# Kernel optimization log

Hardware: AMD Instinct MI355X
Metric: run time of the kernel (lower is better)

Reference implementation:

```python
import jax, jax.numpy as jnp
import numpy as np

K = 20  # kNN fan-out


def knn_idx(x, k):
    # x: (B, C, N). Negative squared pairwise distance; top-k largest = nearest.
    inner = -2.0 * jnp.einsum('bcn,bcm->bnm', x, x)        # (B, N, N)
    xx = jnp.sum(x * x, axis=1)                            # (B, N)
    pd = -xx[:, :, None] - inner - xx[:, None, :]          # (B, N, N)
    return jax.lax.top_k(pd, k)[1]                         # (B, N, k) int32


def get_graph_feature(x, k):
    # x: (B, C, N) -> edge features (B, 2C, N, k)
    idx = knn_idx(x, k)                                    # (B, N, k)
    xt = jnp.transpose(x, (0, 2, 1))                       # (B, N, C)
    nbrs = jax.vmap(lambda pts, ids: pts[ids])(xt, idx)    # (B, N, k, C)
    center = xt[:, :, None, :]                             # (B, N, 1, C)
    feat = jnp.concatenate(
        [nbrs - center, jnp.broadcast_to(center, nbrs.shape)], axis=-1)  # (B,N,k,2C)
    return jnp.transpose(feat, (0, 3, 1, 2))               # (B, 2C, N, k)


def vn_layer(W, x):
    # W: (out, in); x: (B, in, N, k) -> (B, out, N, k)
    return jnp.einsum('oi,bink->bonk', W, x)


def setup_inputs() -> dict:
    key = jax.random.key(0)
    ks = jax.random.split(key, 6)
    B, C, N = 16, 3, 2048
    num_classes = 10
    return {
        'x': jax.random.normal(ks[0], (B, C, N), dtype=jnp.float32),
        'W1': jax.random.normal(ks[1], (64, 6), dtype=jnp.float32),
        'W2': jax.random.normal(ks[2], (128, 64), dtype=jnp.float32),
        'W3': jax.random.normal(ks[3], (256, 128), dtype=jnp.float32),
        'fc_w': jax.random.normal(ks[4], (num_classes, 256), dtype=jnp.float32) * 0.0625,
        'fc_b': jax.random.normal(ks[5], (num_classes,), dtype=jnp.float32) * 0.0625,
    }


def reference(x, W1, W2, W3, fc_w, fc_b):
    h = get_graph_feature(x, K)          # (B, 6, N, k)
    h = vn_layer(W1, h)                  # (B, 64, N, k)
    h = jax.nn.relu(vn_layer(W2, h))     # (B, 128, N, k)
    h = jax.nn.relu(vn_layer(W3, h))     # (B, 256, N, k)
    h = jnp.max(h, axis=-1)              # max over neighbors k -> (B, 256, N)
    h = jnp.max(h, axis=-1)              # global max over points -> (B, 256)
    return h @ fc_w.T + fc_b             # (B, num_classes)
```

## Files before the change

kernel.cpp:

```cpp
#include <hip/hip_runtime.h>
#include <stdint.h>

typedef _Float16 v8h __attribute__((ext_vector_type(8)));
typedef _Float16 v2h __attribute__((ext_vector_type(2)));
typedef float v4f __attribute__((ext_vector_type(4)));

#define NPTS 2048
#define BATCH 16
#define KNN 20
#define PAIRS (NPTS * KNN)

__device__ __forceinline__ unsigned pair_relu_h2(unsigned pu, unsigned qu) {
  v2h a = *(const v2h*)&pu;
  v2h b = *(const v2h*)&qu;
  v2h s = a + b;
  v2h z = {(_Float16)0.f, (_Float16)0.f};
  v2h r = __builtin_elementwise_max(s, z);
  return *(const unsigned*)&r;
}

__global__ void prep_kernel(const float* __restrict__ W1, const float* __restrict__ W2,
                            float* __restrict__ M2a, float* __restrict__ M2b,
                            int* __restrict__ H) {
  if (blockIdx.x == 0 && threadIdx.x < 128) {
    int o = threadIdx.x;
    float a0 = 0, a1 = 0, a2 = 0, b0 = 0, b1 = 0, b2 = 0;
    for (int i = 0; i < 64; ++i) {
      float w2 = W2[o * 64 + i];
      const float* w1r = W1 + i * 6;
      a0 += w2 * w1r[0]; a1 += w2 * w1r[1]; a2 += w2 * w1r[2];
      b0 += w2 * (w1r[3] - w1r[0]); b1 += w2 * (w1r[4] - w1r[1]); b2 += w2 * (w1r[5] - w1r[2]);
    }
    M2a[o * 3 + 0] = a0; M2a[o * 3 + 1] = a1; M2a[o * 3 + 2] = a2;
    M2b[o * 3 + 0] = b0; M2b[o * 3 + 1] = b1; M2b[o * 3 + 2] = b2;
  }
  int g = blockIdx.x * 128 + threadIdx.x;
  if (g < BATCH * 256) H[g] = 0;
}

__global__ __launch_bounds__(64) void pq_kernel(const float* __restrict__ x,
                                                const float* __restrict__ M2a,
                                                const float* __restrict__ M2b,
                                                unsigned short* __restrict__ p,
                                                unsigned short* __restrict__ q) {
  int b = blockIdx.x >> 6;
  int j0 = (blockIdx.x & 63) << 5;
  int t = threadIdx.x;
  int o0 = t * 2;
  float a00 = M2a[o0 * 3 + 0], a01 = M2a[o0 * 3 + 1], a02 = M2a[o0 * 3 + 2];
  float a10 = M2a[o0 * 3 + 3], a11 = M2a[o0 * 3 + 4], a12 = M2a[o0 * 3 + 5];
  float b00 = M2b[o0 * 3 + 0], b01 = M2b[o0 * 3 + 1], b02 = M2b[o0 * 3 + 2];
  float b10 = M2b[o0 * 3 + 3], b11 = M2b[o0 * 3 + 4], b12 = M2b[o0 * 3 + 5];
  const float* xb = x + b * 3 * NPTS;
  unsigned* pw = (unsigned*)p;
  unsigned* qw = (unsigned*)q;
  for (int jj = 0; jj < 32; ++jj) {
    int j = j0 + jj;
    float x0 = xb[j], x1 = xb[NPTS + j], x2 = xb[2 * NPTS + j];
    float p0 = a00 * x0 + a01 * x1 + a02 * x2;
    float p1 = a10 * x0 + a11 * x1 + a12 * x2;
    float q0 = b00 * x0 + b01 * x1 + b02 * x2;
    float q1 = b10 * x0 + b11 * x1 + b12 * x2;
    size_t base = ((size_t)(b * NPTS + j)) * 64 + t;
    auto hp = __builtin_amdgcn_cvt_pkrtz(p0, p1);
    auto hq = __builtin_amdgcn_cvt_pkrtz(q0, q1);
    pw[base] = *(const unsigned*)&hp;
    qw[base] = *(const unsigned*)&hq;
  }
}

__global__ __launch_bounds__(256) void knn_kernel(const float* __restrict__ x,
                                                  int* __restrict__ idxOut) {
  __shared__ float px[NPTS], py[NPTS], pz[NPTS];
  __shared__ unsigned long long cand[4][4][128];
  int b = blockIdx.x >> 7;
  int qblk = blockIdx.x & 127;
  const float* xb = x + b * 3 * NPTS;
  for (int i = threadIdx.x; i < NPTS; i += 256) {
    px[i] = xb[i]; py[i] = xb[NPTS + i]; pz[i] = xb[2 * NPTS + i];
  }
  __syncthreads();
  int wid = threadIdx.x >> 6, lane = threadIdx.x & 63;
  int qbase = qblk * 16 + wid * 4;

  float qx[4], qy[4], qz[4], mn[4];
#pragma unroll
  for (int g = 0; g < 4; ++g) {
    qx[g] = px[qbase + g]; qy[g] = py[qbase + g]; qz[g] = pz[qbase + g];
    mn[g] = 1e30f;
  }

  for (int s = 0; s < 32; ++s) {
    int i = s * 64 + lane;
    float X = px[i], Y = py[i], Z = pz[i];
#pragma unroll
    for (int g = 0; g < 4; ++g) {
      float dx = X - qx[g], dy = Y - qy[g], dz = Z - qz[g];
      mn[g] = fminf(mn[g], dx * dx + dy * dy + dz * dz);
    }
  }

  float tau[4];
#pragma unroll
  for (int g = 0; g < 4; ++g) {
    float v = mn[g];
    for (int k = 2; k <= 64; k <<= 1) {
      for (int j = k >> 1; j > 0; j >>= 1) {
        float o = __shfl_xor(v, j);
        bool low = (lane & j) == 0;
        bool up = (lane & k) == 0;
        v = (low == up) ? fminf(v, o) : fmaxf(v, o);
      }
    }
    tau[g] = __shfl(v, 19) * (1.0f + 3.8e-6f);
  }

  int cnt[4] = {0, 0, 0, 0};
  for (int s = 0; s < 32; ++s) {
    int i = s * 64 + lane;
    float X = px[i], Y = py[i], Z = pz[i];
#pragma unroll
    for (int g = 0; g < 4; ++g) {
      float dx = X - qx[g], dy = Y - qy[g], dz = Z - qz[g];
      float d = dx * dx + dy * dy + dz * dz;
      bool take = d <= tau[g];
      unsigned long long mb = __ballot(take);
      if (take) {
        int pos = cnt[g] + __popcll(mb & ((1ull << lane) - 1ull));
        if (pos < 128)
          cand[wid][g][pos] =
              (((unsigned long long)__float_as_uint(d)) << 32) | (unsigned)i;
      }
      cnt[g] += __popcll(mb);
    }
  }

#pragma unroll
  for (int g = 0; g < 4; ++g) {
    int nc = cnt[g] < 128 ? cnt[g] : 128;
    unsigned long long k0 = (lane < nc) ? cand[wid][g][lane] : ~0ull;
    unsigned long long k1 = (lane + 64 < nc) ? cand[wid][g][lane + 64] : ~0ull;
    int r0 = 0, r1 = 0;
    for (int i = 0; i < nc; ++i) {
      unsigned long long ki = cand[wid][g][i];
      r0 += (ki < k0) ? 1 : 0;
      r1 += (ki < k1) ? 1 : 0;
    }
    long long obase = ((long long)b * NPTS + qbase + g) * KNN;
    if (lane < nc && r0 < KNN) idxOut[obase + r0] = (int)(k0 & 0xffffffffu);
    if (lane + 64 < nc && r1 < KNN) idxOut[obase + r1] = (int)(k1 & 0xffffffffu);
  }
}

__global__ __launch_bounds__(256, 2) void gemm_max_kernel(
    const unsigned short* __restrict__ p, const unsigned short* __restrict__ q,
    const int* __restrict__ idx, const float* __restrict__ W3, int* __restrict__ H) {
  __shared__ __align__(16) unsigned short h2s[2][16 * 136];

  int b = blockIdx.x & 15;
  int w = blockIdx.x >> 4;
  int t = threadIdx.x;
  int lane = t & 63, wid = t >> 6;
  int r16 = lane & 15, quad = lane >> 4;

  v8h bfr[4][4];
#pragma unroll
  for (int ntl = 0; ntl < 4; ++ntl) {
#pragma unroll
    for (int kk = 0; kk < 4; ++kk) {
      int n = (wid * 4 + ntl) * 16 + r16;
      const float* src = W3 + n * 128 + kk * 32 + quad * 8;
      v8h f;
#pragma unroll
      for (int jj = 0; jj < 8; ++jj)
        f[jj] = (_Float16)src[jj];
      bfr[ntl][kk] = f;
    }
  }

  const unsigned short* pB = p + (size_t)b * NPTS * 128;
  const unsigned short* qB = q + (size_t)b * NPTS * 128;
  const int* idxB = idx + (size_t)b * PAIRS;

  int pm = t >> 4;
  int cseg = t & 15;

  uint4 P4n, Q4n;
  {
    int pr = w * 16 + pm;
    int n0 = pr / 20;
    int j0 = idxB[pr] & (NPTS - 1);
    P4n = *(const uint4*)(pB + (size_t)j0 * 128 + cseg * 8);
    Q4n = *(const uint4*)(qB + (size_t)n0 * 128 + cseg * 8);
  }

  float vmx[4] = {0.f, 0.f, 0.f, 0.f};
  int buf = 0;
  for (int T = w; T < PAIRS / 16; T += 96) {
    uint4 R;
    R.x = pair_relu_h2(P4n.x, Q4n.x);
    R.y = pair_relu_h2(P4n.y, Q4n.y);
    R.z = pair_relu_h2(P4n.z, Q4n.z);
    R.w = pair_relu_h2(P4n.w, Q4n.w);
    *(uint4*)&h2s[buf][pm * 136 + cseg * 8] = R;
    __syncthreads();

    int Tn = T + 96;
    if (Tn < PAIRS / 16) {
      int prn = Tn * 16 + pm;
      int nn = prn / 20;
      int jn = idxB[prn] & (NPTS - 1);
      P4n = *(const uint4*)(pB + (size_t)jn * 128 + cseg * 8);
      Q4n = *(const uint4*)(qB + (size_t)nn * 128 + cseg * 8);
    }

    v8h a[4];
#pragma unroll
    for (int kk = 0; kk < 4; ++kk)
      a[kk] = *(const v8h*)&h2s[buf][r16 * 136 + kk * 32 + quad * 8];

#pragma unroll
    for (int ntl = 0; ntl < 4; ++ntl) {
      v4f acc = {0.f, 0.f, 0.f, 0.f};
#pragma unroll
      for (int kk = 0; kk < 4; ++kk)
        acc = __builtin_amdgcn_mfma_f32_16x16x32_f16(a[kk], bfr[ntl][kk], acc, 0, 0, 0);
      vmx[ntl] = fmaxf(vmx[ntl], fmaxf(fmaxf(acc[0], acc[1]), fmaxf(acc[2], acc[3])));
    }
    buf ^= 1;
  }

#pragma unroll
  for (int ntl = 0; ntl < 4; ++ntl) {
    float vv = vmx[ntl];
    vv = fmaxf(vv, __shfl_xor(vv, 16));
    vv = fmaxf(vv, __shfl_xor(vv, 32));
    if (quad == 0) {
      int ch = (wid * 4 + ntl) * 16 + r16;
      atomicMax(&H[b * 256 + ch], __float_as_int(vv));
    }
  }
}

__global__ __launch_bounds__(64) void fc_kernel(const int* __restrict__ Hi,
                                                const float* __restrict__ fcw,
                                                const float* __restrict__ fcb,
                                                float* __restrict__ out) {
  int b = blockIdx.x / 10, r = blockIdx.x % 10;
  int lane = threadIdx.x;
  const float* Hb = (const float*)Hi + b * 256;
  float s = 0.f;
#pragma unroll
  for (int c = lane; c < 256; c += 64) s += Hb[c] * fcw[r * 256 + c];
#pragma unroll
  for (int m = 32; m > 0; m >>= 1) s += __shfl_xor(s, m);
  if (lane == 0) out[b * 10 + r] = s + fcb[r];
}

extern "C" void kernel_launch(void* const* d_in, const int* in_sizes, int n_in,
                              void* d_out, int out_size, void* d_ws, size_t ws_size,
                              hipStream_t stream) {
  const float* x   = (const float*)d_in[0];
  const float* W1  = (const float*)d_in[1];
  const float* W2  = (const float*)d_in[2];
  const float* W3  = (const float*)d_in[3];
  const float* fcw = (const float*)d_in[4];
  const float* fcb = (const float*)d_in[5];
  float* out = (float*)d_out;
  char* ws = (char*)d_ws;

  float* M2a = (float*)(ws + 0);
  float* M2b = (float*)(ws + 1536);
  int* H     = (int*)(ws + 4096);
  int* idx   = (int*)(ws + 24576);
  unsigned short* p = (unsigned short*)(ws + 3145728);
  unsigned short* q = (unsigned short*)(ws + 12582912);

  prep_kernel<<<32, 128, 0, stream>>>(W1, W2, M2a, M2b, H);
  pq_kernel<<<BATCH * 64, 64, 0, stream>>>(x, M2a, M2b, p, q);
  knn_kernel<<<BATCH * 128, 256, 0, stream>>>(x, idx);
  gemm_max_kernel<<<BATCH * 96, 256, 0, stream>>>(p, q, idx, W3, H);
  fc_kernel<<<BATCH * 10, 64, 0, stream>>>(H, fcw, fcb, out);
}
```

Baseline: 188.4 us.

## Use 32x32x16 MFMA with 512-thread blocks and swizzled LDS tile

Restructures the gather-GEMM-max kernel to issue 32x32x16 f16 MFMAs instead of 16x16x32. Each block now has 8 waves covering all 256 output channels for 32 pairs per step, and there are 32 blocks per batch instead of 96. The unpadded LDS tile uses an XOR swizzle to avoid bank conflicts. This gives fewer MFMA instructions and larger per-step tiles, but the grid is smaller and there is one barrier per 32-pair step across 512 threads.

```diff
diff --git a/kernel.cpp b/kernel.cpp
--- a/kernel.cpp
+++ b/kernel.cpp
@@ -4,6 +4,7 @@
 typedef _Float16 v8h __attribute__((ext_vector_type(8)));
 typedef _Float16 v2h __attribute__((ext_vector_type(2)));
 typedef float v4f __attribute__((ext_vector_type(4)));
+typedef float v16f __attribute__((ext_vector_type(16)));
 
 #define NPTS 2048
 #define BATCH 16
@@ -152,30 +153,25 @@
   }
 }
 
-__global__ __launch_bounds__(256, 2) void gemm_max_kernel(
+__global__ __launch_bounds__(512, 4) void gemm_max_kernel(
     const unsigned short* __restrict__ p, const unsigned short* __restrict__ q,
     const int* __restrict__ idx, const float* __restrict__ W3, int* __restrict__ H) {
-  __shared__ __align__(16) unsigned short h2s[2][16 * 136];
-
-  int b = blockIdx.x & 15;
-  int w = blockIdx.x >> 4;
+  __shared__ __align__(16) unsigned short h2s[2][32 * 128];
+
+  int b = blockIdx.x >> 5;
+  int w = blockIdx.x & 31;
   int t = threadIdx.x;
   int lane = t & 63, wid = t >> 6;
-  int r16 = lane & 15, quad = lane >> 4;
-
-  v8h bfr[4][4];
-#pragma unroll
-  for (int ntl = 0; ntl < 4; ++ntl) {
-#pragma unroll
-    for (int kk = 0; kk < 4; ++kk) {
-      int n = (wid * 4 + ntl) * 16 + r16;
-      const float* src = W3 + n * 128 + kk * 32 + quad * 8;
-      v8h f;
-#pragma unroll
-      for (int jj = 0; jj < 8; ++jj)
-        f[jj] = (_Float16)src[jj];
-      bfr[ntl][kk] = f;
-    }
+  int col = lane & 31, hi = lane >> 5;
+
+  v8h bfr[8];
+#pragma unroll
+  for (int kk = 0; kk < 8; ++kk) {
+    const float* src = W3 + (size_t)(wid * 32 + col) * 128 + kk * 16 + hi * 8;
+    v8h f;
+#pragma unroll
+    for (int jj = 0; jj < 8; ++jj) f[jj] = (_Float16)src[jj];
+    bfr[kk] = f;
   }
 
   const unsigned short* pB = p + (size_t)b * NPTS * 128;
@@ -184,61 +180,55 @@
 
   int pm = t >> 4;
   int cseg = t & 15;
+  int stoff = pm * 128 + ((cseg ^ (pm & 7)) * 8);
 
   uint4 P4n, Q4n;
   {
-    int pr = w * 16 + pm;
+    int pr = w * 32 + pm;
     int n0 = pr / 20;
     int j0 = idxB[pr] & (NPTS - 1);
     P4n = *(const uint4*)(pB + (size_t)j0 * 128 + cseg * 8);
     Q4n = *(const uint4*)(qB + (size_t)n0 * 128 + cseg * 8);
   }
 
-  float vmx[4] = {0.f, 0.f, 0.f, 0.f};
+  float vmx = 0.f;
   int buf = 0;
-  for (int T = w; T < PAIRS / 16; T += 96) {
+  for (int T = w; T < PAIRS / 32; T += 32) {
     uint4 R;
     R.x = pair_relu_h2(P4n.x, Q4n.x);
     R.y = pair_relu_h2(P4n.y, Q4n.y);
     R.z = pair_relu_h2(P4n.z, Q4n.z);
     R.w = pair_relu_h2(P4n.w, Q4n.w);
-    *(uint4*)&h2s[buf][pm * 136 + cseg * 8] = R;
+    *(uint4*)&h2s[buf][stoff] = R;
     __syncthreads();
 
-    int Tn = T + 96;
-    if (Tn < PAIRS / 16) {
-      int prn = Tn * 16 + pm;
+    int Tn = T + 32;
+    if (Tn < PAIRS / 32) {
+      int prn = Tn * 32 + pm;
       int nn = prn / 20;
       int jn = idxB[prn] & (NPTS - 1);
       P4n = *(const uint4*)(pB + (size_t)jn * 128 + cseg * 8);
       Q4n = *(const uint4*)(qB + (size_t)nn * 128 + cseg * 8);
     }
 
-    v8h a[4];
-#pragma unroll
-    for (int kk = 0; kk < 4; ++kk)
-      a[kk] = *(const v8h*)&h2s[buf][r16 * 136 + kk * 32 + quad * 8];
-
-#pragma unroll
-    for (int ntl = 0; ntl < 4; ++ntl) {
-      v4f acc = {0.f, 0.f, 0.f, 0.f};
-#pragma unroll
-      for (int kk = 0; kk < 4; ++kk)
-        acc = __builtin_amdgcn_mfma_f32_16x16x32_f16(a[kk], bfr[ntl][kk], acc, 0, 0, 0);
-      vmx[ntl] = fmaxf(vmx[ntl], fmaxf(fmaxf(acc[0], acc[1]), fmaxf(acc[2], acc[3])));
-    }
+    v16f acc = {0.f};
+#pragma unroll
+    for (int kk = 0; kk < 8; ++kk) {
+      v8h a = *(const v8h*)&h2s[buf][col * 128 + (((kk * 2 + hi) ^ (col & 7)) * 8)];
+      acc = __builtin_amdgcn_mfma_f32_32x32x16_f16(a, bfr[kk], acc, 0, 0, 0);
+    }
+    float m0 = fmaxf(fmaxf(acc[0], acc[1]), fmaxf(acc[2], acc[3]));
+    float m1 = fmaxf(fmaxf(acc[4], acc[5]), fmaxf(acc[6], acc[7]));
+    float m2 = fmaxf(fmaxf(acc[8], acc[9]), fmaxf(acc[10], acc[11]));
+    float m3 = fmaxf(fmaxf(acc[12], acc[13]), fmaxf(acc[14], acc[15]));
+    vmx = fmaxf(vmx, fmaxf(fmaxf(m0, m1), fmaxf(m2, m3)));
     buf ^= 1;
   }
 
-#pragma unroll
-  for (int ntl = 0; ntl < 4; ++ntl) {
-    float vv = vmx[ntl];
-    vv = fmaxf(vv, __shfl_xor(vv, 16));
-    vv = fmaxf(vv, __shfl_xor(vv, 32));
-    if (quad == 0) {
-      int ch = (wid * 4 + ntl) * 16 + r16;
-      atomicMax(&H[b * 256 + ch], __float_as_int(vv));
-    }
+  float vv = fmaxf(vmx, __shfl_xor(vmx, 32));
+  if (hi == 0) {
+    int ch = wid * 32 + col;
+    atomicMax(&H[b * 256 + ch], __float_as_int(vv));
   }
 }
 
@@ -279,6 +269,6 @@
   prep_kernel<<<32, 128, 0, stream>>>(W1, W2, M2a, M2b, H);
   pq_kernel<<<BATCH * 64, 64, 0, stream>>>(x, M2a, M2b, p, q);
   knn_kernel<<<BATCH * 128, 256, 0, stream>>>(x, idx);
-  gemm_max_kernel<<<BATCH * 96, 256, 0, stream>>>(p, q, idx, W3, H);
+  gemm_max_kernel<<<BATCH * 32, 512, 0, stream>>>(p, q, idx, W3, H);
   fc_kernel<<<BATCH * 10, 64, 0, stream>>>(H, fcw, fcb, out);
 }
```

After: 177.4 us. 5.8% less time.
